# Optimization experiments

Measured on AMD Instinct MI355X. Metric: run time of the kernel, lower is better.

Reference implementation:

```python
import jax, jax.numpy as jnp
import numpy as np

B, F_IN, NCH, T = 1, 1, 1536, 128
NW = [476, 476, 292]          # wires per plane (face 0)
NC = [10000, 10000, 10000]    # crossings per plane pair (01, 12, 20)
NCROSS = sum(NC)
E = 120000                    # ~4 nearest-neighbor edges per crossing node
N_FEAT_WIRE = 4
OUT_CH = 4
NODE_DIM = 2 * (F_IN + N_FEAT_WIRE) + 3  # = 13, matches GAT input dim


def setup_inputs() -> dict:
    key = jax.random.key(0)
    ks = jax.random.split(key, 18)
    x = jax.random.normal(ks[0], (B, F_IN, NCH, T), jnp.float32)
    chan_p0 = jax.random.randint(ks[1], (NW[0],), 0, NCH, jnp.int32)
    chan_p1 = jax.random.randint(ks[2], (NW[1],), 0, NCH, jnp.int32)
    chan_p2 = jax.random.randint(ks[3], (NW[2],), 0, NCH, jnp.int32)
    gidx_01 = jax.random.randint(ks[4], (NC[0], 2), 0, min(NW[0], NW[1]), jnp.int32)
    gidx_12 = jax.random.randint(ks[5], (NC[1], 2), 0, min(NW[1], NW[2]), jnp.int32)
    gidx_20 = jax.random.randint(ks[6], (NC[2], 2), 0, min(NW[2], NW[0]), jnp.int32)
    ray_01 = jax.random.normal(ks[7], (NC[0], 2), jnp.float32)
    ray_12 = jax.random.normal(ks[8], (NC[1], 2), jnp.float32)
    ray_20 = jax.random.normal(ks[9], (NC[2], 2), jnp.float32)
    edges = jax.random.randint(ks[10], (2, E), 0, NCROSS, jnp.int32)
    W_gat = jax.random.normal(ks[11], (NODE_DIM, OUT_CH), jnp.float32) * 0.1
    a_src = jax.random.normal(ks[12], (OUT_CH,), jnp.float32) * 0.1
    a_dst = jax.random.normal(ks[13], (OUT_CH,), jnp.float32) * 0.1
    b_gat = jnp.zeros((OUT_CH,), jnp.float32)
    W_mlp = jax.random.normal(ks[14], (OUT_CH, 1), jnp.float32) * 0.1
    b_mlp = jnp.zeros((1,), jnp.float32)
    return dict(x=x, chan_p0=chan_p0, chan_p1=chan_p1, chan_p2=chan_p2,
                gidx_01=gidx_01, gidx_12=gidx_12, gidx_20=gidx_20,
                ray_01=ray_01, ray_12=ray_12, ray_20=ray_20, edges=edges,
                W_gat=W_gat, a_src=a_src, a_dst=a_dst, b_gat=b_gat,
                W_mlp=W_mlp, b_mlp=b_mlp)


def _plane_feats(x, chan, plane_id):
    # x: [B,F,C,T] -> per-wire features [B,T,Nw,F+4]:
    # (signal, wire_ident, channel, 0, plane_id) -- mirrors as_wires_f0_pX.
    sig = jnp.transpose(x[:, :, chan, :], (0, 3, 2, 1))  # [B,T,Nw,F]
    nw = chan.shape[0]
    wire_id = jnp.arange(nw, dtype=jnp.float32)
    extra = jnp.stack([wire_id, chan.astype(jnp.float32),
                       jnp.zeros(nw, jnp.float32),
                       jnp.full((nw,), plane_id, jnp.float32)], axis=-1)  # [Nw,4]
    extra = jnp.broadcast_to(extra[None, None], sig.shape[:2] + extra.shape)
    return jnp.concatenate([sig, extra], axis=-1)


def _cross(fA, fB, gidx, rc):
    # crossing node features: wireA feats ++ wireB feats ++ ray xy ++ tick
    n = gidx.shape[0]
    tick = jnp.broadcast_to(jnp.arange(T, dtype=jnp.float32)[None, :, None, None],
                            (B, T, n, 1))
    rcb = jnp.broadcast_to(rc[None, None], (B, T, n, 2))
    return jnp.concatenate([fA[:, :, gidx[:, 0]], fB[:, :, gidx[:, 1]], rcb, tick],
                           axis=-1)  # [B,T,n,13]


def _gat_one(h, a_src, a_dst, src, dst):
    # single-graph, single-head GAT attention + aggregation. h: [N,OUT_CH]
    s = h @ a_src  # [N]
    d = h @ a_dst
    e = jax.nn.leaky_relu(s[src] + d[dst], 0.2)  # [E]
    m = jax.ops.segment_max(e, dst, num_segments=NCROSS)
    m = jnp.where(jnp.isfinite(m), m, 0.0)
    w = jnp.exp(e - m[dst])
    denom = jax.ops.segment_sum(w, dst, num_segments=NCROSS)
    msg = jax.ops.segment_sum(w[:, None] * h[src], dst, num_segments=NCROSS)
    return msg / (denom[:, None] + 1e-9)


def reference(x, chan_p0, chan_p1, chan_p2, gidx_01, gidx_12, gidx_20,
              ray_01, ray_12, ray_20, edges,
              W_gat, a_src, a_dst, b_gat, W_mlp, b_mlp):
    f0 = _plane_feats(x, chan_p0, 0.0)
    f1 = _plane_feats(x, chan_p1, 1.0)
    f2 = _plane_feats(x, chan_p2, 2.0)
    nodes = jnp.concatenate([_cross(f0, f1, gidx_01, ray_01),
                             _cross(f1, f2, gidx_12, ray_12),
                             _cross(f2, f0, gidx_20, ray_20)], axis=2)  # [B,T,N,13]
    h = nodes @ W_gat + b_gat  # [B,T,N,OUT_CH]
    src, dst = edges[0], edges[1]
    gat = jax.vmap(jax.vmap(lambda hh: _gat_one(hh, a_src, a_dst, src, dst)))
    g = gat(h)  # [B,T,N,OUT_CH]
    return jax.nn.sigmoid(g @ W_mlp + b_mlp)  # [B,T,N,1]
```

## Files before the change

kernel.cpp:

```cpp
#include <hip/hip_runtime.h>

#define T_TICKS 128
#define NCPAIR  10000
#define NCROSS  30000
#define E_EDGES 120000
#define TG      4
#define NTG     (T_TICKS / TG)
#define NBLK_N  ((NCROSS + 255) / 256)
#define CAP     32
#define EPB     ((E_EDGES + NBLK_N - 1) / NBLK_N)


__global__ void k_feat(const float* __restrict__ x,
                       const int* __restrict__ c0, const int* __restrict__ c1,
                       const int* __restrict__ c2,
                       const int* __restrict__ g01, const int* __restrict__ g12,
                       const int* __restrict__ g20,
                       const float* __restrict__ r01,
                       const float* __restrict__ r12,
                       const float* __restrict__ r20,
                       const float* __restrict__ Wg,
                       const float* __restrict__ bg,
                       const float* __restrict__ as_,
                       const float* __restrict__ ad_,
                       const float* __restrict__ Wm,
                       const int* __restrict__ e_src,
                       const int* __restrict__ e_dst,
                       int* __restrict__ counts, int* __restrict__ bucket,
                       float4* __restrict__ sp4, float4* __restrict__ dv4) {
    const int tid = threadIdx.x;
    const int tg8 = blockIdx.y;
    if (tg8 == 0) {
        const int lo = blockIdx.x * EPB;
        const int hi = min(lo + EPB, E_EDGES);
        for (int i = lo + tid; i < hi; i += 256) {
            const int s = e_src[i];
            const int d = e_dst[i];
            const int slot = atomicAdd(&counts[d], 1);
            if (slot < CAP) bucket[(size_t)d * CAP + slot] = s;
        }
    }
    const int n = blockIdx.x * 256 + tid;
    if (n >= NCROSS) return;

    int iA, iB, m;
    float pA, pB;
    const int* cA;
    const int* cB;
    const float* ray;
    if (n < NCPAIR) {
        m = n; cA = c0; cB = c1; pA = 0.f; pB = 1.f; ray = r01;
        iA = g01[2 * m]; iB = g01[2 * m + 1];
    } else if (n < 2 * NCPAIR) {
        m = n - NCPAIR; cA = c1; cB = c2; pA = 1.f; pB = 2.f; ray = r12;
        iA = g12[2 * m]; iB = g12[2 * m + 1];
    } else {
        m = n - 2 * NCPAIR; cA = c2; cB = c0; pA = 2.f; pB = 0.f; ray = r20;
        iA = g20[2 * m]; iB = g20[2 * m + 1];
    }
    const int chA = cA[iA];
    const int chB = cB[iB];
    const float rx = ray[2 * m];
    const float ry = ray[2 * m + 1];

    float base[4];
#pragma unroll
    for (int c = 0; c < 4; c++) {
        base[c] = bg[c]
                + (float)iA  * Wg[1 * 4 + c] + (float)chA * Wg[2 * 4 + c]
                + pA         * Wg[4 * 4 + c]
                + (float)iB  * Wg[6 * 4 + c] + (float)chB * Wg[7 * 4 + c]
                + pB         * Wg[9 * 4 + c]
                + rx         * Wg[10 * 4 + c] + ry * Wg[11 * 4 + c];
    }
    float sB = 0, dB = 0, pBs = 0;
    float sA1 = 0, dA1 = 0, pA1 = 0;
    float sB1 = 0, dB1 = 0, pB1 = 0;
    float sT = 0, dT = 0, pT = 0;
#pragma unroll
    for (int c = 0; c < 4; c++) {
        const float va = as_[c], vd = ad_[c], vm = Wm[c];
        sB  += base[c] * va;  dB  += base[c] * vd;  pBs += base[c] * vm;
        sA1 += Wg[c] * va;    dA1 += Wg[c] * vd;    pA1 += Wg[c] * vm;
        sB1 += Wg[5*4+c]*va;  dB1 += Wg[5*4+c]*vd;  pB1 += Wg[5*4+c]*vm;
        sT  += Wg[12*4+c]*va; dT  += Wg[12*4+c]*vd; pT  += Wg[12*4+c]*vm;
    }

#pragma unroll
    for (int half = 0; half < 2; half++) {
        const int tg4 = tg8 * 2 + half;
        const float4 xa = *(const float4*)(x + chA * T_TICKS + tg4 * TG);
        const float4 xb = *(const float4*)(x + chB * T_TICKS + tg4 * TG);
        const float sa[4] = {xa.x, xa.y, xa.z, xa.w};
        const float sb[4] = {xb.x, xb.y, xb.z, xb.w};
        float sv[4], dvv[4], pv[4];
#pragma unroll
        for (int k = 0; k < TG; k++) {
            const float tk = (float)(tg4 * TG + k);
            sv[k]  = sB  + sa[k]*sA1 + sb[k]*sB1 + tk*sT;
            dvv[k] = dB  + sa[k]*dA1 + sb[k]*dB1 + tk*dT;
            pv[k]  = pBs + sa[k]*pA1 + sb[k]*pB1 + tk*pT;
        }
        const size_t rec = (size_t)tg4 * NCROSS + n;
        sp4[rec * 2]     = make_float4(sv[0], pv[0], sv[1], pv[1]);
        sp4[rec * 2 + 1] = make_float4(sv[2], pv[2], sv[3], pv[3]);
        dv4[rec]         = make_float4(dvv[0], dvv[1], dvv[2], dvv[3]);
    }
}


__device__ __forceinline__ void upd(float& mx, float& den, float& p,
                                    const float e, const float pj) {
    const float dif = e - mx;
    const float ex = __expf(-fabsf(dif));
    const bool g = dif > 0.f;
    const float scale = g ? ex : 1.f;
    const float w = g ? 1.f : ex;
    mx = g ? e : mx;
    den = fmaf(den, scale, w);
    p = fmaf(p, scale, w * pj);
}

__device__ __forceinline__ void edge_upd(const float4 f0, const float4 f1,
                                         const float* dd, float* mx,
                                         float* den, float* pa) {
    float e0 = f0.x + dd[0]; e0 = fmaxf(e0, 0.2f * e0);
    upd(mx[0], den[0], pa[0], e0, f0.y);
    float e1 = f0.z + dd[1]; e1 = fmaxf(e1, 0.2f * e1);
    upd(mx[1], den[1], pa[1], e1, f0.w);
    float e2 = f1.x + dd[2]; e2 = fmaxf(e2, 0.2f * e2);
    upd(mx[2], den[2], pa[2], e2, f1.y);
    float e3 = f1.z + dd[3]; e3 = fmaxf(e3, 0.2f * e3);
    upd(mx[3], den[3], pa[3], e3, f1.w);
}

__global__ void k_gat(const float4* __restrict__ sp4,
                      const float4* __restrict__ dv4,
                      const int* __restrict__ counts,
                      const int* __restrict__ bucket,
                      const float* __restrict__ bm,
                      float* __restrict__ out) {
    const int lid = blockIdx.x;
    const int xcd = lid & 7;
    const int s   = lid >> 3;
    const int q   = s / NBLK_N;
    const int nb  = s - q * NBLK_N;
    const int tg  = xcd + 8 * q;
    const int bbase = nb * 256;
    const int tid = threadIdx.x;
    const int wsz = min(256, NCROSS - bbase);

    __shared__ int perm[256];
    __shared__ int bins[CAP + 1];
    __shared__ int boff[CAP + 1];
    __shared__ float lres[TG][257];

    int deg0 = 0;
    if (tid < wsz) deg0 = min(counts[bbase + tid], CAP);
    if (tid <= CAP) bins[tid] = 0;
    __syncthreads();
    int lp = 0;
    if (tid < wsz) lp = atomicAdd(&bins[deg0], 1);
    __syncthreads();
    if (tid == 0) {
        int run = 0;
        for (int d = CAP; d >= 0; d--) { boff[d] = run; run += bins[d]; }
    }
    __syncthreads();
    if (tid < wsz) perm[boff[deg0] + lp] = tid;
    __syncthreads();

    if (tid < wsz) {
        const int nloc = perm[tid];
        const int n = bbase + nloc;
        const int deg = min(counts[n], CAP);
        const int* bkt = bucket + (size_t)n * CAP;

        const float4* spb = sp4 + (size_t)tg * NCROSS * 2;
        const float4 dvv = dv4[(size_t)tg * NCROSS + n];
        const float dd[TG] = {dvv.x, dvv.y, dvv.z, dvv.w};

        float mx[TG], den[TG], pa[TG];
#pragma unroll
        for (int k = 0; k < TG; k++) { mx[k] = -INFINITY; den[k] = 0.f; pa[k] = 0.f; }

        int j = 0;
        for (; j + 2 <= deg; j += 2) {
            const int s0 = bkt[j];
            const int s1 = bkt[j + 1];
            const float4 f0 = spb[(size_t)s0 * 2];
            const float4 f1 = spb[(size_t)s0 * 2 + 1];
            const float4 f2 = spb[(size_t)s1 * 2];
            const float4 f3 = spb[(size_t)s1 * 2 + 1];
            edge_upd(f0, f1, dd, mx, den, pa);
            edge_upd(f2, f3, dd, mx, den, pa);
        }
        if (j < deg) {
            const int s0 = bkt[j];
            const float4 f0 = spb[(size_t)s0 * 2];
            const float4 f1 = spb[(size_t)s0 * 2 + 1];
            edge_upd(f0, f1, dd, mx, den, pa);
        }

        const float bb = bm[0];
#pragma unroll
        for (int k = 0; k < TG; k++) {
            const float logit = pa[k] / (den[k] + 1e-9f) + bb;
            lres[k][nloc] = 1.f / (1.f + __expf(-logit));
        }
    }
    __syncthreads();
    if (tid < wsz) {
#pragma unroll
        for (int k = 0; k < TG; k++) {
            out[(size_t)(tg * TG + k) * NCROSS + bbase + tid] = lres[k][tid];
        }
    }
}


extern "C" void kernel_launch(void* const* d_in, const int* in_sizes, int n_in,
                              void* d_out, int out_size, void* d_ws, size_t ws_size,
                              hipStream_t stream) {
    const float* x   = (const float*)d_in[0];
    const int* c0  = (const int*)d_in[1];
    const int* c1  = (const int*)d_in[2];
    const int* c2  = (const int*)d_in[3];
    const int* g01 = (const int*)d_in[4];
    const int* g12 = (const int*)d_in[5];
    const int* g20 = (const int*)d_in[6];
    const float* r01 = (const float*)d_in[7];
    const float* r12 = (const float*)d_in[8];
    const float* r20 = (const float*)d_in[9];
    const int* edges = (const int*)d_in[10];
    const float* Wg  = (const float*)d_in[11];
    const float* as_ = (const float*)d_in[12];
    const float* ad_ = (const float*)d_in[13];
    const float* bg  = (const float*)d_in[14];
    const float* Wm  = (const float*)d_in[15];
    const float* bm  = (const float*)d_in[16];
    float* out = (float*)d_out;

    const int* e_src = edges;
    const int* e_dst = edges + E_EDGES;

    char* ws = (char*)d_ws;
    size_t off = 0;
    int* counts  = (int*)(ws + off); off += NCROSS * sizeof(int);
    off = (off + 63) & ~(size_t)63;
    int* bucket  = (int*)(ws + off); off += (size_t)NCROSS * CAP * sizeof(int);
    off = (off + 255) & ~(size_t)255;
    float4* sp4  = (float4*)(ws + off); off += (size_t)NTG * NCROSS * 32;
    float4* dv4  = (float4*)(ws + off); off += (size_t)NTG * NCROSS * 16;
    (void)ws_size; (void)n_in; (void)in_sizes; (void)out_size;

    hipMemsetAsync(counts, 0, NCROSS * sizeof(int), stream);

    dim3 gridF(NBLK_N, 16);
    k_feat<<<gridF, 256, 0, stream>>>(x, c0, c1, c2, g01, g12, g20,
                                      r01, r12, r20, Wg, bg, as_, ad_, Wm,
                                      e_src, e_dst, counts, bucket, sp4, dv4);
    k_gat<<<NBLK_N * NTG, 256, 0, stream>>>(sp4, dv4, counts, bucket, bm, out);
}
```

Before: 150.8 us.

## Recompute per-tick node features in GAT kernel from LDS-staged signal slice

Instead of materialising per-tick source/dest/projection values for every node and tick group in global memory, the prep kernel now stores only tick-independent per-node constants (with channel indices) plus a transposed copy of the signal. The GAT kernel stages the signal slice for its tick group in shared memory and recomputes the per-edge score and projection on the fly. The edge bucket is also transposed for coalesced neighbor-index reads, the edge scatter runs as flat extra threads in the prep kernel, and the block size grows to 512. This trades a large global write/read of intermediates for extra ALU work and LDS gathers, with higher shared-memory use per block.

Result: faster. 136.1 us (-9.7%).

```diff
diff --git a/kernel.cpp b/kernel.cpp
--- a/kernel.cpp
+++ b/kernel.cpp
@@ -1,17 +1,20 @@
 #include <hip/hip_runtime.h>
 
 #define T_TICKS 128
+#define NCH     1536
 #define NCPAIR  10000
 #define NCROSS  30000
 #define E_EDGES 120000
 #define TG      4
 #define NTG     (T_TICKS / TG)
-#define NBLK_N  ((NCROSS + 255) / 256)
 #define CAP     32
-#define EPB     ((E_EDGES + NBLK_N - 1) / NBLK_N)
-
-
-__global__ void k_feat(const float* __restrict__ x,
+#define BN      512
+#define NBLK    ((NCROSS + BN - 1) / BN)
+#define NXPOS   (NTG * NCH)
+#define PREP_ITEMS (NCROSS + E_EDGES + NXPOS)
+
+
+__global__ void k_prep(const float* __restrict__ x,
                        const int* __restrict__ c0, const int* __restrict__ c1,
                        const int* __restrict__ c2,
                        const int* __restrict__ g01, const int* __restrict__ g12,
@@ -26,85 +29,64 @@
                        const float* __restrict__ Wm,
                        const int* __restrict__ e_src,
                        const int* __restrict__ e_dst,
-                       int* __restrict__ counts, int* __restrict__ bucket,
-                       float4* __restrict__ sp4, float4* __restrict__ dv4) {
-    const int tid = threadIdx.x;
-    const int tg8 = blockIdx.y;
-    if (tg8 == 0) {
-        const int lo = blockIdx.x * EPB;
-        const int hi = min(lo + EPB, E_EDGES);
-        for (int i = lo + tid; i < hi; i += 256) {
-            const int s = e_src[i];
-            const int d = e_dst[i];
-            const int slot = atomicAdd(&counts[d], 1);
-            if (slot < CAP) bucket[(size_t)d * CAP + slot] = s;
-        }
-    }
-    const int n = blockIdx.x * 256 + tid;
-    if (n >= NCROSS) return;
-
-    int iA, iB, m;
-    float pA, pB;
-    const int* cA;
-    const int* cB;
-    const float* ray;
-    if (n < NCPAIR) {
-        m = n; cA = c0; cB = c1; pA = 0.f; pB = 1.f; ray = r01;
-        iA = g01[2 * m]; iB = g01[2 * m + 1];
-    } else if (n < 2 * NCPAIR) {
-        m = n - NCPAIR; cA = c1; cB = c2; pA = 1.f; pB = 2.f; ray = r12;
-        iA = g12[2 * m]; iB = g12[2 * m + 1];
-    } else {
-        m = n - 2 * NCPAIR; cA = c2; cB = c0; pA = 2.f; pB = 0.f; ray = r20;
-        iA = g20[2 * m]; iB = g20[2 * m + 1];
-    }
-    const int chA = cA[iA];
-    const int chB = cB[iB];
-    const float rx = ray[2 * m];
-    const float ry = ray[2 * m + 1];
-
-    float base[4];
-#pragma unroll
-    for (int c = 0; c < 4; c++) {
-        base[c] = bg[c]
-                + (float)iA  * Wg[1 * 4 + c] + (float)chA * Wg[2 * 4 + c]
-                + pA         * Wg[4 * 4 + c]
-                + (float)iB  * Wg[6 * 4 + c] + (float)chB * Wg[7 * 4 + c]
-                + pB         * Wg[9 * 4 + c]
-                + rx         * Wg[10 * 4 + c] + ry * Wg[11 * 4 + c];
-    }
-    float sB = 0, dB = 0, pBs = 0;
-    float sA1 = 0, dA1 = 0, pA1 = 0;
-    float sB1 = 0, dB1 = 0, pB1 = 0;
-    float sT = 0, dT = 0, pT = 0;
-#pragma unroll
-    for (int c = 0; c < 4; c++) {
-        const float va = as_[c], vd = ad_[c], vm = Wm[c];
-        sB  += base[c] * va;  dB  += base[c] * vd;  pBs += base[c] * vm;
-        sA1 += Wg[c] * va;    dA1 += Wg[c] * vd;    pA1 += Wg[c] * vm;
-        sB1 += Wg[5*4+c]*va;  dB1 += Wg[5*4+c]*vd;  pB1 += Wg[5*4+c]*vm;
-        sT  += Wg[12*4+c]*va; dT  += Wg[12*4+c]*vd; pT  += Wg[12*4+c]*vm;
-    }
-
-#pragma unroll
-    for (int half = 0; half < 2; half++) {
-        const int tg4 = tg8 * 2 + half;
-        const float4 xa = *(const float4*)(x + chA * T_TICKS + tg4 * TG);
-        const float4 xb = *(const float4*)(x + chB * T_TICKS + tg4 * TG);
-        const float sa[4] = {xa.x, xa.y, xa.z, xa.w};
-        const float sb[4] = {xb.x, xb.y, xb.z, xb.w};
-        float sv[4], dvv[4], pv[4];
-#pragma unroll
-        for (int k = 0; k < TG; k++) {
-            const float tk = (float)(tg4 * TG + k);
-            sv[k]  = sB  + sa[k]*sA1 + sb[k]*sB1 + tk*sT;
-            dvv[k] = dB  + sa[k]*dA1 + sb[k]*dB1 + tk*dT;
-            pv[k]  = pBs + sa[k]*pA1 + sb[k]*pB1 + tk*pT;
-        }
-        const size_t rec = (size_t)tg4 * NCROSS + n;
-        sp4[rec * 2]     = make_float4(sv[0], pv[0], sv[1], pv[1]);
-        sp4[rec * 2 + 1] = make_float4(sv[2], pv[2], sv[3], pv[3]);
-        dv4[rec]         = make_float4(dvv[0], dvv[1], dvv[2], dvv[3]);
+                       int* __restrict__ counts,
+                       int* __restrict__ bucketT,
+                       float4* __restrict__ c4,
+                       float* __restrict__ dBv,
+                       float4* __restrict__ xT4) {
+    const int gid = blockIdx.x * 256 + threadIdx.x;
+    if (gid < NCROSS) {
+        const int n = gid;
+        int iA, iB, m;
+        float pA, pB;
+        const int* cA;
+        const int* cB;
+        const float* ray;
+        if (n < NCPAIR) {
+            m = n; cA = c0; cB = c1; pA = 0.f; pB = 1.f; ray = r01;
+            iA = g01[2 * m]; iB = g01[2 * m + 1];
+        } else if (n < 2 * NCPAIR) {
+            m = n - NCPAIR; cA = c1; cB = c2; pA = 1.f; pB = 2.f; ray = r12;
+            iA = g12[2 * m]; iB = g12[2 * m + 1];
+        } else {
+            m = n - 2 * NCPAIR; cA = c2; cB = c0; pA = 2.f; pB = 0.f; ray = r20;
+            iA = g20[2 * m]; iB = g20[2 * m + 1];
+        }
+        const int chA = cA[iA];
+        const int chB = cB[iB];
+        const float rx = ray[2 * m];
+        const float ry = ray[2 * m + 1];
+
+        float base[4];
+#pragma unroll
+        for (int c = 0; c < 4; c++) {
+            base[c] = bg[c]
+                    + (float)iA  * Wg[1 * 4 + c] + (float)chA * Wg[2 * 4 + c]
+                    + pA         * Wg[4 * 4 + c]
+                    + (float)iB  * Wg[6 * 4 + c] + (float)chB * Wg[7 * 4 + c]
+                    + pB         * Wg[9 * 4 + c]
+                    + rx         * Wg[10 * 4 + c] + ry * Wg[11 * 4 + c];
+        }
+        float sB = 0.f, dB = 0.f, pBs = 0.f;
+#pragma unroll
+        for (int c = 0; c < 4; c++) {
+            sB  = fmaf(base[c], as_[c], sB);
+            dB  = fmaf(base[c], ad_[c], dB);
+            pBs = fmaf(base[c], Wm[c], pBs);
+        }
+        c4[n]  = make_float4(sB, pBs, __int_as_float(chA), __int_as_float(chB));
+        dBv[n] = dB;
+    } else if (gid < NCROSS + E_EDGES) {
+        const int i = gid - NCROSS;
+        const int s = e_src[i];
+        const int d = e_dst[i];
+        const int slot = atomicAdd(&counts[d], 1);
+        if (slot < CAP) bucketT[slot * NCROSS + d] = s;
+    } else if (gid < PREP_ITEMS) {
+        const int i = gid - (NCROSS + E_EDGES);
+        const int tg = i / NCH;
+        const int c = i - tg * NCH;
+        xT4[i] = *(const float4*)(x + c * T_TICKS + tg * TG);
     }
 }
 
@@ -121,39 +103,66 @@
     p = fmaf(p, scale, w * pj);
 }
 
-__device__ __forceinline__ void edge_upd(const float4 f0, const float4 f1,
-                                         const float* dd, float* mx,
-                                         float* den, float* pa) {
-    float e0 = f0.x + dd[0]; e0 = fmaxf(e0, 0.2f * e0);
-    upd(mx[0], den[0], pa[0], e0, f0.y);
-    float e1 = f0.z + dd[1]; e1 = fmaxf(e1, 0.2f * e1);
-    upd(mx[1], den[1], pa[1], e1, f0.w);
-    float e2 = f1.x + dd[2]; e2 = fmaxf(e2, 0.2f * e2);
-    upd(mx[2], den[2], pa[2], e2, f1.y);
-    float e3 = f1.z + dd[3]; e3 = fmaxf(e3, 0.2f * e3);
-    upd(mx[3], den[3], pa[3], e3, f1.w);
-}
-
-__global__ void k_gat(const float4* __restrict__ sp4,
-                      const float4* __restrict__ dv4,
-                      const int* __restrict__ counts,
-                      const int* __restrict__ bucket,
-                      const float* __restrict__ bm,
-                      float* __restrict__ out) {
+__device__ __forceinline__ void edge_proc(const float4 cs, const float4* xs,
+                                          const float sA1, const float sB1,
+                                          const float pA1, const float pB1,
+                                          const float* ts, const float* tp,
+                                          const float* dd,
+                                          float* mx, float* den, float* pa) {
+    const float4 a4 = xs[__float_as_int(cs.z)];
+    const float4 b4 = xs[__float_as_int(cs.w)];
+    const float a[4] = {a4.x, a4.y, a4.z, a4.w};
+    const float b[4] = {b4.x, b4.y, b4.z, b4.w};
+#pragma unroll
+    for (int k = 0; k < TG; k++) {
+        const float sv = cs.x + a[k] * sA1 + b[k] * sB1 + ts[k];
+        const float pv = cs.y + a[k] * pA1 + b[k] * pB1 + tp[k];
+        float e = sv + dd[k];
+        e = fmaxf(e, 0.2f * e);
+        upd(mx[k], den[k], pa[k], e, pv);
+    }
+}
+
+__global__ __launch_bounds__(512, 8) void k_gat(
+        const float4* __restrict__ xT4,
+        const float4* __restrict__ c4,
+        const float* __restrict__ dBv,
+        const int* __restrict__ counts,
+        const int* __restrict__ bucketT,
+        const float* __restrict__ Wg,
+        const float* __restrict__ as_,
+        const float* __restrict__ ad_,
+        const float* __restrict__ Wm,
+        const float* __restrict__ bm,
+        float* __restrict__ out) {
     const int lid = blockIdx.x;
     const int xcd = lid & 7;
     const int s   = lid >> 3;
-    const int q   = s / NBLK_N;
-    const int nb  = s - q * NBLK_N;
+    const int q   = s / NBLK;
+    const int nb  = s - q * NBLK;
     const int tg  = xcd + 8 * q;
-    const int bbase = nb * 256;
+    const int bbase = nb * BN;
     const int tid = threadIdx.x;
-    const int wsz = min(256, NCROSS - bbase);
-
-    __shared__ int perm[256];
+    const int wsz = min(BN, NCROSS - bbase);
+
+    __shared__ float4 xs[NCH];
+    __shared__ int perm[BN];
     __shared__ int bins[CAP + 1];
     __shared__ int boff[CAP + 1];
-    __shared__ float lres[TG][257];
+    __shared__ float lres[TG][BN];
+
+    for (int c = tid; c < NCH; c += BN) xs[c] = xT4[tg * NCH + c];
+
+    float sA1 = 0, dA1 = 0, pA1 = 0, sB1 = 0, dB1 = 0, pB1 = 0,
+          sT = 0, dT = 0, pT = 0;
+#pragma unroll
+    for (int c = 0; c < 4; c++) {
+        const float va = as_[c], vd = ad_[c], vm = Wm[c];
+        const float w0 = Wg[c], w5 = Wg[5 * 4 + c], w12 = Wg[12 * 4 + c];
+        sA1 = fmaf(w0, va, sA1);  dA1 = fmaf(w0, vd, dA1);  pA1 = fmaf(w0, vm, pA1);
+        sB1 = fmaf(w5, va, sB1);  dB1 = fmaf(w5, vd, dB1);  pB1 = fmaf(w5, vm, pB1);
+        sT  = fmaf(w12, va, sT);  dT  = fmaf(w12, vd, dT);  pT  = fmaf(w12, vm, pT);
+    }
 
     int deg0 = 0;
     if (tid < wsz) deg0 = min(counts[bbase + tid], CAP);
@@ -174,32 +183,40 @@
         const int nloc = perm[tid];
         const int n = bbase + nloc;
         const int deg = min(counts[n], CAP);
-        const int* bkt = bucket + (size_t)n * CAP;
-
-        const float4* spb = sp4 + (size_t)tg * NCROSS * 2;
-        const float4 dvv = dv4[(size_t)tg * NCROSS + n];
-        const float dd[TG] = {dvv.x, dvv.y, dvv.z, dvv.w};
-
+
+        const float4 cc = c4[n];
+        const float4 a4 = xs[__float_as_int(cc.z)];
+        const float4 b4 = xs[__float_as_int(cc.w)];
+        const float dB = dBv[n];
+        const float a[4] = {a4.x, a4.y, a4.z, a4.w};
+        const float b[4] = {b4.x, b4.y, b4.z, b4.w};
+
+        float dd[TG], ts[TG], tp[TG];
+#pragma unroll
+        for (int k = 0; k < TG; k++) {
+            const float tk = (float)(tg * TG + k);
+            dd[k] = dB + a[k] * dA1 + b[k] * dB1 + tk * dT;
+            ts[k] = tk * sT;
+            tp[k] = tk * pT;
+        }
         float mx[TG], den[TG], pa[TG];
 #pragma unroll
         for (int k = 0; k < TG; k++) { mx[k] = -INFINITY; den[k] = 0.f; pa[k] = 0.f; }
 
+        const int* bk = bucketT + n;
         int j = 0;
         for (; j + 2 <= deg; j += 2) {
-            const int s0 = bkt[j];
-            const int s1 = bkt[j + 1];
-            const float4 f0 = spb[(size_t)s0 * 2];
-            const float4 f1 = spb[(size_t)s0 * 2 + 1];
-            const float4 f2 = spb[(size_t)s1 * 2];
-            const float4 f3 = spb[(size_t)s1 * 2 + 1];
-            edge_upd(f0, f1, dd, mx, den, pa);
-            edge_upd(f2, f3, dd, mx, den, pa);
+            const int s0 = bk[j * NCROSS];
+            const int s1 = bk[(j + 1) * NCROSS];
+            const float4 cs0 = c4[s0];
+            const float4 cs1 = c4[s1];
+            edge_proc(cs0, xs, sA1, sB1, pA1, pB1, ts, tp, dd, mx, den, pa);
+            edge_proc(cs1, xs, sA1, sB1, pA1, pB1, ts, tp, dd, mx, den, pa);
         }
         if (j < deg) {
-            const int s0 = bkt[j];
-            const float4 f0 = spb[(size_t)s0 * 2];
-            const float4 f1 = spb[(size_t)s0 * 2 + 1];
-            edge_upd(f0, f1, dd, mx, den, pa);
+            const int s0 = bk[j * NCROSS];
+            const float4 cs0 = c4[s0];
+            edge_proc(cs0, xs, sA1, sB1, pA1, pB1, ts, tp, dd, mx, den, pa);
         }
 
         const float bb = bm[0];
@@ -246,19 +263,23 @@
 
     char* ws = (char*)d_ws;
     size_t off = 0;
-    int* counts  = (int*)(ws + off); off += NCROSS * sizeof(int);
-    off = (off + 63) & ~(size_t)63;
-    int* bucket  = (int*)(ws + off); off += (size_t)NCROSS * CAP * sizeof(int);
-    off = (off + 255) & ~(size_t)255;
-    float4* sp4  = (float4*)(ws + off); off += (size_t)NTG * NCROSS * 32;
-    float4* dv4  = (float4*)(ws + off); off += (size_t)NTG * NCROSS * 16;
+    int* counts = (int*)(ws + off); off += NCROSS * sizeof(int);
+    off = (off + 255) & ~(size_t)255;
+    int* bucketT = (int*)(ws + off); off += (size_t)CAP * NCROSS * sizeof(int);
+    off = (off + 255) & ~(size_t)255;
+    float4* c4 = (float4*)(ws + off); off += (size_t)NCROSS * sizeof(float4);
+    off = (off + 255) & ~(size_t)255;
+    float* dBv = (float*)(ws + off); off += NCROSS * sizeof(float);
+    off = (off + 255) & ~(size_t)255;
+    float4* xT4 = (float4*)(ws + off); off += (size_t)NXPOS * sizeof(float4);
     (void)ws_size; (void)n_in; (void)in_sizes; (void)out_size;
 
     hipMemsetAsync(counts, 0, NCROSS * sizeof(int), stream);
 
-    dim3 gridF(NBLK_N, 16);
-    k_feat<<<gridF, 256, 0, stream>>>(x, c0, c1, c2, g01, g12, g20,
-                                      r01, r12, r20, Wg, bg, as_, ad_, Wm,
-                                      e_src, e_dst, counts, bucket, sp4, dv4);
-    k_gat<<<NBLK_N * NTG, 256, 0, stream>>>(sp4, dv4, counts, bucket, bm, out);
-}
+    k_prep<<<(PREP_ITEMS + 255) / 256, 256, 0, stream>>>(
+        x, c0, c1, c2, g01, g12, g20, r01, r12, r20, Wg, bg, as_, ad_, Wm,
+        e_src, e_dst, counts, bucketT, c4, dBv, xT4);
+
+    k_gat<<<NBLK * NTG, BN, 0, stream>>>(xT4, c4, dBv, counts, bucketT,
+                                         Wg, as_, ad_, Wm, bm, out);
+}
```
